# Kernel tuning notes

Measured on AMD Instinct MI355X. Metric: run time of the kernel, lower is better.

## Reference

```python
import jax, jax.numpy as jnp
import numpy as np

N = 10000   # num_nodes
F = 64      # latent_dim
U = 128     # num_units
B = 8       # batch
K = 2       # gcn_step
E = 160000  # edges (avg degree 16)
M = 2 * K + 1  # num_matrices = len(supports)*gcn_step + 1


def setup_inputs() -> dict:
    rng = np.random.default_rng(0)
    rows = rng.integers(0, N, E).astype(np.int32)
    cols = rng.integers(0, N, E).astype(np.int32)
    vals = (rng.random(E).astype(np.float32) + 0.1)
    # random-walk normalization D^{-1} A, per the original utils.calculate_random_walk_matrix
    deg_out = np.zeros(N, np.float32); np.add.at(deg_out, rows, vals)
    deg_in = np.zeros(N, np.float32); np.add.at(deg_in, cols, vals)
    # support1 = (D_out^{-1} A)^T : out[c] += vals/d_out[r] * x[r]  -> dst=cols, src=rows
    w1 = vals / np.maximum(deg_out[rows], 1e-8)
    # support2 = (D_in^{-1} A^T)^T : out[r] += vals/d_in[c] * x[c]  -> dst=rows, src=cols
    w2 = vals / np.maximum(deg_in[cols], 1e-8)

    key = jax.random.key(0)
    ks = jax.random.split(key, 4)

    def xavier(k, shape):
        std = (2.0 / (shape[0] + shape[1])) ** 0.5
        return jax.random.normal(k, shape, jnp.float32) * std

    return {
        'y': jax.random.normal(ks[0], (B, N * F), jnp.float32),
        'W_lat': xavier(ks[1], (M * F, F)),
        'b_lat': jnp.ones((F,), jnp.float32),   # bias_start=1.0, shared (keyed by length)
        'W_units': xavier(ks[2], (M * F, U)),
        'b_units': jnp.zeros((U,), jnp.float32),
        'W_final': xavier(ks[3], (M * U, F)),
        'sup1_w': jnp.asarray(w1),
        'sup2_w': jnp.asarray(w2),
        'edge_rows': jnp.asarray(rows),
        'edge_cols': jnp.asarray(cols),
    }


def _spmm(dst, src, w, x):
    # sparse matmul S @ x with S given as COO edge list; x: (N, Fin, B)
    return jax.ops.segment_sum(w[:, None, None] * x[src], dst, num_segments=N)


def _gconv(x, supports, W, b):
    # x: (B, N, Fin) -> (B, N*Fout); Chebyshev diffusion convolution
    Bsz, n, fin = x.shape
    x0 = jnp.transpose(x, (1, 2, 0))  # (N, Fin, B)
    xs = [x0]
    for dst, src, w in supports:
        xk_2 = x0
        x1 = _spmm(dst, src, w, x0)
        xs.append(x1)
        for _ in range(2, K + 1):
            x2 = 2.0 * _spmm(dst, src, w, x1) - xk_2
            xs.append(x2)
            xk_2, x1 = x1, x2
    X = jnp.stack(xs, axis=-1)                       # (N, Fin, B, M)
    X = jnp.transpose(X, (2, 0, 1, 3)).reshape(Bsz * n, fin * len(xs))  # feature-major, matrix-minor
    out = X @ W + b
    return out.reshape(Bsz, n * W.shape[1])


def reference(y, W_lat, b_lat, W_units, b_units, W_final, sup1_w, sup2_w, edge_rows, edge_cols):
    supports = [(edge_cols, edge_rows, sup1_w), (edge_rows, edge_cols, sup2_w)]
    x = y.reshape(B, N, F)
    # theta gate (bias_start=1.0 via shared b_lat)
    theta = jax.nn.sigmoid(_gconv(x, supports, W_lat, b_lat))
    # ode_func_net: gen_layers=1 hidden gconv + final gconv (final bias is shared b_lat!)
    c = jnp.tanh(_gconv(x, supports, W_units, b_units)).reshape(B, N, U)
    c = jnp.tanh(_gconv(c, supports, W_final, b_lat))
    return -theta * c
```

## Files before the change

kernel.cpp:

```cpp
#include <hip/hip_runtime.h>

#define N_NODES 10000
#define NEDGE 160000
#define NB 80000
#define EPAD (NEDGE + 8 * N_NODES)

typedef unsigned int u32;
typedef unsigned short u16;
typedef __attribute__((ext_vector_type(8))) short short8;
typedef __attribute__((ext_vector_type(4))) float float4v;

__device__ __forceinline__ u16 f2bf(float f) {
    u32 u = __float_as_uint(f);
    return (u16)((u + 0x7fffu + ((u >> 16) & 1u)) >> 16);
}
__device__ __forceinline__ float lo16(u32 u) { return __uint_as_float(u << 16); }
__device__ __forceinline__ float hi16(u32 u) { return __uint_as_float(u & 0xffff0000u); }
__device__ __forceinline__ u32 pack2(float a, float b) {
    return (u32)f2bf(a) | (((u32)f2bf(b)) << 16);
}
__device__ __forceinline__ float fast_tanh(float v) {
    return 1.f - 2.f / (__expf(2.f * v) + 1.f);
}

static const size_t SLAB = (size_t)NB * 64;

__global__ __launch_bounds__(256) void prepcount_kernel(
    const float2* __restrict__ y, u32* __restrict__ X0,
    const float* __restrict__ W_lat, const float* __restrict__ W_units,
    u16* __restrict__ bpk12, const float* __restrict__ W_final, u16* __restrict__ bpkP,
    const int* __restrict__ rows, const int* __restrict__ cols, int* __restrict__ cnt) {
    int b = blockIdx.x, t = threadIdx.x;
    if (b < 10000) {
        int idx = b * 256 + t;
        int fh = idx & 31;
        int rb = idx >> 5;
        int bb = rb & 7;
        int n = rb >> 3;
        float2 v = y[((size_t)bb * N_NODES + n) * 32 + fh];
        X0[idx] = pack2(v.x, v.y);
    } else if (b < 10240) {
        int idx = (b - 10000) * 256 + t;
        int j = idx & 7;
        int lane = (idx >> 3) & 63;
        int rest = idx >> 9;
        int ct = rest % 12;
        int ks = rest / 12;
        int k = ks * 32 + (lane >> 4) * 8 + j;
        int col = ct * 16 + (lane & 15);
        int wrow = (k % 64) * 5 + (k / 64);
        float v = (col < 64) ? W_lat[wrow * 64 + col] : W_units[wrow * 128 + (col - 64)];
        bpk12[idx] = f2bf(v);
    } else if (b < 10400) {
        int idx = (b - 10240) * 256 + t;
        int j8 = idx & 7;
        int lane = (idx >> 3) & 63;
        int rest = idx >> 9;
        int ct = rest % 20;
        int ks = rest / 20;
        int k = ks * 32 + (lane >> 4) * 8 + j8;
        int col = ct * 16 + (lane & 15);
        int slot = col >> 6, j = col & 63;
        float v;
        if (slot == 0)
            v = W_final[(k * 5 + 0) * 64 + j] - W_final[(k * 5 + 2) * 64 + j] -
                W_final[(k * 5 + 4) * 64 + j];
        else
            v = W_final[(k * 5 + slot) * 64 + j];
        bpkP[idx] = f2bf(v);
    } else {
        int e = (b - 10400) * 256 + t;
        atomicAdd(&cnt[cols[e]], 1);
        atomicAdd(&cnt[N_NODES + rows[e]], 1);
    }
}

__global__ void blocksum_kernel(const int* __restrict__ cnt, int* __restrict__ bsums) {
    __shared__ int red[4];
    int arr = blockIdx.x / 40;
    int c = blockIdx.x % 40;
    int idx = c * 256 + threadIdx.x;
    int v = (idx < N_NODES) ? ((cnt[arr * N_NODES + idx] + 7) & ~7) : 0;
#pragma unroll
    for (int off = 32; off; off >>= 1) v += __shfl_down(v, off, 64);
    int wv = threadIdx.x >> 6, ln = threadIdx.x & 63;
    if (ln == 0) red[wv] = v;
    __syncthreads();
    if (threadIdx.x == 0) bsums[blockIdx.x] = red[0] + red[1] + red[2] + red[3];
}

__global__ void scanapply_kernel(int* __restrict__ cnt, const int* __restrict__ bsums,
                                 int* __restrict__ rowptr1, int* __restrict__ rowptr2) {
    __shared__ int lds[256];
    int arr = blockIdx.x / 40;
    int c = blockIdx.x % 40;
    int base = 0;
    for (int i = 0; i < c; i++) base += bsums[arr * 40 + i];
    int idx = c * 256 + threadIdx.x;
    bool ok = idx < N_NODES;
    int v = ok ? ((cnt[arr * N_NODES + idx] + 7) & ~7) : 0;
    int t = threadIdx.x;
    lds[t] = v;
    __syncthreads();
    for (int off = 1; off < 256; off <<= 1) {
        int add = (t >= off) ? lds[t - off] : 0;
        __syncthreads();
        lds[t] += add;
        __syncthreads();
    }
    int excl = lds[t] - v + base;
    if (ok) {
        int* rp = arr ? rowptr2 : rowptr1;
        rp[idx] = excl;
        cnt[arr * N_NODES + idx] = excl;
    }
    if (c == 39 && t == 255) {
        (arr ? rowptr2 : rowptr1)[N_NODES] = base + lds[255];
    }
}

__global__ void scatter_kernel(const int* __restrict__ rows, const int* __restrict__ cols,
                               const float* __restrict__ w1, const float* __restrict__ w2,
                               int* __restrict__ cur1, int* __restrict__ cur2,
                               int2* __restrict__ edges1, int2* __restrict__ edges2) {
    int e = blockIdx.x * 256 + threadIdx.x;
    if (e < NEDGE) {
        int r = rows[e], c = cols[e];
        int p1 = atomicAdd(&cur1[c], 1);
        edges1[p1] = make_int2(r, __float_as_int(w1[e]));
        int p2 = atomicAdd(&cur2[r], 1);
        edges2[p2] = make_int2(c, __float_as_int(w2[e]));
    }
}

__device__ __forceinline__ void gacc(float* acc, float w, uint4 u) {
    acc[0] += w * lo16(u.x); acc[1] += w * hi16(u.x);
    acc[2] += w * lo16(u.y); acc[3] += w * hi16(u.y);
    acc[4] += w * lo16(u.z); acc[5] += w * hi16(u.z);
    acc[6] += w * lo16(u.w); acc[7] += w * hi16(u.w);
}

__device__ __forceinline__ void gather_sliced(const u32* __restrict__ Xin,
                                              const int* __restrict__ rp,
                                              const int2* __restrict__ eg,
                                              int row, bool valid, int su, int l,
                                              float* acc) {
    int e = 0, e1 = 0;
    if (valid) {
        e = rp[row] + l;
        e1 = rp[row + 1];
    }
    while (__ballot(e < e1)) {
        int2 me = make_int2(0, 0);
        if (e < e1) me = eg[e];
#pragma unroll
        for (int j = 0; j < 8; j++) {
            int s = __shfl(me.x, j, 8);
            float w = __int_as_float(__shfl(me.y, j, 8));
            uint4 u = *(const uint4*)(Xin + (size_t)s * 256 + su + l * 4);
            gacc(acc, w, u);
        }
        e += 8;
    }
}

__global__ __launch_bounds__(256) void spmm2_kernel(
    const u32* __restrict__ XinA, const u32* __restrict__ XprevA, u32* __restrict__ XoutA,
    const u32* __restrict__ XinB, const u32* __restrict__ XprevB, u32* __restrict__ XoutB,
    const int* __restrict__ rowptr1, const int2* __restrict__ edges1,
    const int* __restrict__ rowptr2, const int2* __restrict__ edges2,
    float alpha, float beta) {
    int t = threadIdx.x;
    int lane = t & 63;
    int g = lane >> 3, l = lane & 7;
    int slice = blockIdx.x & 7;
    int chunk = blockIdx.x >> 3;
    int su = slice * 32;
    int v = chunk * 32 + (t >> 6) * 8 + g;
    bool hB = v >= N_NODES;
    int n = hB ? v - N_NODES : v;
    const u32* Xin = hB ? XinB : XinA;
    const u32* Xprev = hB ? XprevB : XprevA;
    u32* Xout = hB ? XoutB : XoutA;
    const int* rp = hB ? rowptr2 : rowptr1;
    const int2* eg = hB ? edges2 : edges1;

    float acc[8] = {0.f, 0.f, 0.f, 0.f, 0.f, 0.f, 0.f, 0.f};
    gather_sliced(Xin, rp, eg, n, true, su, l, acc);

    size_t o = (size_t)n * 256 + su + l * 4;
    if (beta != 0.f) {
        uint4 p = *(const uint4*)(Xprev + o);
        acc[0] = alpha * acc[0] + beta * lo16(p.x); acc[1] = alpha * acc[1] + beta * hi16(p.x);
        acc[2] = alpha * acc[2] + beta * lo16(p.y); acc[3] = alpha * acc[3] + beta * hi16(p.y);
        acc[4] = alpha * acc[4] + beta * lo16(p.z); acc[5] = alpha * acc[5] + beta * hi16(p.z);
        acc[6] = alpha * acc[6] + beta * lo16(p.w); acc[7] = alpha * acc[7] + beta * hi16(p.w);
    } else {
#pragma unroll
        for (int i = 0; i < 8; i++) acc[i] *= alpha;
    }
    uint4 r;
    r.x = pack2(acc[0], acc[1]);
    r.y = pack2(acc[2], acc[3]);
    r.z = pack2(acc[4], acc[5]);
    r.w = pack2(acc[6], acc[7]);
    *(uint4*)(Xout + o) = r;
}

__global__ __launch_bounds__(256) void spmm_final_kernel(
    const u32* __restrict__ T1, const u32* __restrict__ T2,
    const u32* __restrict__ Q, const u32* __restrict__ theta,
    const int* __restrict__ rowptr1, const int2* __restrict__ edges1,
    const int* __restrict__ rowptr2, const int2* __restrict__ edges2,
    float* __restrict__ outF) {
    int t = threadIdx.x;
    int lane = t & 63;
    int g = lane >> 3, l = lane & 7;
    int slice = blockIdx.x & 7;
    int chunk = blockIdx.x >> 3;
    int su = slice * 32;
    int n = chunk * 32 + (t >> 6) * 8 + g;
    bool valid = n < N_NODES;

    float acc[8] = {0.f, 0.f, 0.f, 0.f, 0.f, 0.f, 0.f, 0.f};
    gather_sliced(T1, rowptr1, edges1, n, valid, su, l, acc);
    gather_sliced(T2, rowptr2, edges2, n, valid, su, l, acc);
    if (!valid) return;

    size_t o = (size_t)n * 256 + su + l * 4;
    uint4 q = *(const uint4*)(Q + o);
    uint4 th = *(const uint4*)(theta + o);
    float res[8];
    res[0] = -lo16(th.x) * fast_tanh(lo16(q.x) + acc[0]);
    res[1] = -hi16(th.x) * fast_tanh(hi16(q.x) + acc[1]);
    res[2] = -lo16(th.y) * fast_tanh(lo16(q.y) + acc[2]);
    res[3] = -hi16(th.y) * fast_tanh(hi16(q.y) + acc[3]);
    res[4] = -lo16(th.z) * fast_tanh(lo16(q.z) + acc[4]);
    res[5] = -hi16(th.z) * fast_tanh(hi16(q.z) + acc[5]);
    res[6] = -lo16(th.w) * fast_tanh(lo16(q.w) + acc[6]);
    res[7] = -hi16(th.w) * fast_tanh(hi16(q.w) + acc[7]);
    float* dst = outF + (size_t)slice * (N_NODES * 64) + (size_t)n * 64 + l * 8;
    *(float4*)(dst) = make_float4(res[0], res[1], res[2], res[3]);
    *(float4*)(dst + 4) = make_float4(res[4], res[5], res[6], res[7]);
}

struct Slabs { const u16* p[5]; };

template <int FIN, int NM, int NOUT, int CT, int MODE>
__global__ __launch_bounds__(256, 6) void gemm_kernel(
    Slabs A, const u16* __restrict__ Bp, const float* __restrict__ bias1,
    const float* __restrict__ bias2, u16* __restrict__ O1, u16* __restrict__ O2) {
    constexpr int K = NM * FIN;
    constexpr int KS = K / 32;
    constexpr int CTT = NOUT / 16;
    static_assert(CT * 4 == CTT, "4 waves cover all col tiles");

    int t = threadIdx.x;
    int lane = t & 63;
    int wave = t >> 6;
    int ctBase = wave * CT;
    int rowBase = blockIdx.x * 32;
    int mrow = lane & 15;
    int kq = lane >> 4;

    float4v acc0[CT], acc1[CT];
#pragma unroll
    for (int c = 0; c < CT; c++) {
        acc0[c] = (float4v){0.f, 0.f, 0.f, 0.f};
        acc1[c] = (float4v){0.f, 0.f, 0.f, 0.f};
    }

#pragma unroll
    for (int ks = 0; ks < KS; ks++) {
        int k = ks * 32 + kq * 8;
        int m = k / FIN;
        int koff = k % FIN;
        const u16* ap = A.p[m];
        short8 a0 = *(const short8*)(ap + (size_t)(rowBase + mrow) * FIN + koff);
        short8 a1 = *(const short8*)(ap + (size_t)(rowBase + 16 + mrow) * FIN + koff);
#pragma unroll
        for (int ct = 0; ct < CT; ct++) {
            short8 b = *(const short8*)(Bp +
                        ((size_t)(ks * CTT + ctBase + ct) * 64 + lane) * 8);
            acc0[ct] = __builtin_amdgcn_mfma_f32_16x16x32_bf16(b, a0, acc0[ct], 0, 0, 0);
            acc1[ct] = __builtin_amdgcn_mfma_f32_16x16x32_bf16(b, a1, acc1[ct], 0, 0, 0);
        }
    }

#pragma unroll
    for (int hr = 0; hr < 2; hr++) {
        size_t r = (size_t)(rowBase + hr * 16 + mrow);
#pragma unroll
        for (int ct = 0; ct < CT; ct++) {
            float4v av = hr ? acc1[ct] : acc0[ct];
            int col0 = (ctBase + ct) * 16 + kq * 4;
            float v[4];
#pragma unroll
            for (int i = 0; i < 4; i++) v[i] = av[i];
            if (MODE == 0) {
                if (col0 < 64) {
#pragma unroll
                    for (int i = 0; i < 4; i++) v[i] += bias1[col0 + i];
                }
                uint2 w = make_uint2(pack2(v[0], v[1]), pack2(v[2], v[3]));
                *(uint2*)(O1 + (size_t)(col0 >> 6) * SLAB + r * 64 + (col0 & 63)) = w;
            } else {
                if (col0 < 64) {
#pragma unroll
                    for (int i = 0; i < 4; i++)
                        v[i] = 1.f / (1.f + __expf(-(v[i] + bias1[col0 + i])));
                    uint2 w = make_uint2(pack2(v[0], v[1]), pack2(v[2], v[3]));
                    *(uint2*)(O1 + r * 64 + col0) = w;
                } else {
#pragma unroll
                    for (int i = 0; i < 4; i++)
                        v[i] = fast_tanh(v[i] + bias2[col0 - 64 + i]);
                    uint2 w = make_uint2(pack2(v[0], v[1]), pack2(v[2], v[3]));
                    *(uint2*)(O2 + r * 128 + (col0 - 64)) = w;
                }
            }
        }
    }
}

extern "C" void kernel_launch(void* const* d_in, const int* in_sizes, int n_in,
                              void* d_out, int out_size, void* d_ws, size_t ws_size,
                              hipStream_t stream) {
    const float2* y    = (const float2*)d_in[0];
    const float* W_lat = (const float*)d_in[1];
    const float* b_lat = (const float*)d_in[2];
    const float* W_units = (const float*)d_in[3];
    const float* b_units = (const float*)d_in[4];
    const float* W_final = (const float*)d_in[5];
    const float* sup1w = (const float*)d_in[6];
    const float* sup2w = (const float*)d_in[7];
    const int* rows    = (const int*)d_in[8];
    const int* cols    = (const int*)d_in[9];
    float* out = (float*)d_out;

    char* ws = (char*)d_ws;
    size_t off = 0;
    auto alloc = [&](size_t bytes) -> void* {
        void* p = ws + off;
        off += (bytes + 511) & ~(size_t)511;
        return p;
    };
    int* rowptr1 = (int*)alloc((N_NODES + 1) * 4);
    int* rowptr2 = (int*)alloc((N_NODES + 1) * 4);
    int* cnt = (int*)alloc((size_t)2 * N_NODES * 4);
    int* bsums = (int*)alloc(80 * 4);
    int2* edges1 = (int2*)alloc((size_t)EPAD * 8);
    int2* edges2 = (int2*)alloc((size_t)EPAD * 8);
    u16* bpk12 = (u16*)alloc((size_t)61440 * 2);
    u16* bpkP = (u16*)alloc((size_t)40960 * 2);
    u16* theta = (u16*)alloc((size_t)NB * 64 * 2);
    u16* S = (u16*)alloc((size_t)5 * NB * 64 * 2);
    u16* H0 = (u16*)alloc((size_t)NB * 128 * 2);
    u16* T1 = (u16*)alloc((size_t)NB * 64 * 2);
    u16* T2 = (u16*)alloc((size_t)NB * 64 * 2);

    hipMemsetAsync(cnt, 0, (size_t)2 * N_NODES * 4, stream);
    hipMemsetAsync(edges1, 0, (size_t)EPAD * 8, stream);
    hipMemsetAsync(edges2, 0, (size_t)EPAD * 8, stream);
    prepcount_kernel<<<11025, 256, 0, stream>>>(y, (u32*)S, W_lat, W_units, bpk12,
                                                W_final, bpkP, rows, cols, cnt);
    blocksum_kernel<<<80, 256, 0, stream>>>(cnt, bsums);
    scanapply_kernel<<<80, 256, 0, stream>>>(cnt, bsums, rowptr1, rowptr2);
    scatter_kernel<<<625, 256, 0, stream>>>(rows, cols, sup1w, sup2w,
                                            cnt, cnt + N_NODES, edges1, edges2);

    const u32* S0 = (const u32*)S;
    u32* X1 = (u32*)(S + 1 * SLAB);
    u32* X2 = (u32*)(S + 2 * SLAB);
    u32* X3 = (u32*)(S + 3 * SLAB);
    u32* X4 = (u32*)(S + 4 * SLAB);
    spmm2_kernel<<<5000, 256, 0, stream>>>(S0, nullptr, X1, S0, nullptr, X3,
                                           rowptr1, edges1, rowptr2, edges2, 1.f, 0.f);
    spmm2_kernel<<<5000, 256, 0, stream>>>(X1, S0, X2, X3, S0, X4,
                                           rowptr1, edges1, rowptr2, edges2, 2.f, -1.f);

    Slabs SX;
    for (int m = 0; m < 5; m++) SX.p[m] = S + (size_t)m * SLAB;
    gemm_kernel<64, 5, 192, 3, 1><<<2500, 256, 0, stream>>>(SX, bpk12, b_lat, b_units, theta, H0);

    Slabs SH;
    SH.p[0] = H0;
    gemm_kernel<128, 1, 320, 5, 0><<<2500, 256, 0, stream>>>(SH, bpkP, b_lat, nullptr, S, nullptr);

    const u32* Q  = (const u32*)(S + 0 * SLAB);
    const u32* P1 = (const u32*)(S + 1 * SLAB);
    const u32* P2 = (const u32*)(S + 2 * SLAB);
    const u32* P3 = (const u32*)(S + 3 * SLAB);
    const u32* P4 = (const u32*)(S + 4 * SLAB);
    spmm2_kernel<<<5000, 256, 0, stream>>>(P2, P1, (u32*)T1, P4, P3, (u32*)T2,
                                           rowptr1, edges1, rowptr2, edges2, 2.f, 1.f);
    spmm_final_kernel<<<2504, 256, 0, stream>>>((const u32*)T1, (const u32*)T2, Q,
                                                (const u32*)theta,
                                                rowptr1, edges1, rowptr2, edges2, out);
}
```

Measured before the change: 334.7 us.

## Restructure GEMM to 16-row tiles with preloaded A and prefetched B fragments

The GEMM kernel now handles 16 rows per block instead of 32, which doubles the grid to 5000 blocks. It preloads every A fragment into registers up front and double-buffers the B fragment loads one k-step ahead of the MFMAs. Launch bounds drop from 6 to 4 blocks per CU to leave room for the larger register footprint. The aim is more parallelism and latency hiding, at the cost of halving B-fragment reuse (each B load now feeds one MFMA instead of two) and lowering occupancy.

Result: slower. 342.7 us (+2.4%).

```diff
diff --git a/kernel.cpp b/kernel.cpp
--- a/kernel.cpp
+++ b/kernel.cpp
@@ -247,77 +247,82 @@
 struct Slabs { const u16* p[5]; };
 
 template <int FIN, int NM, int NOUT, int CT, int MODE>
-__global__ __launch_bounds__(256, 6) void gemm_kernel(
+__global__ __launch_bounds__(256, 4) void gemm_kernel(
     Slabs A, const u16* __restrict__ Bp, const float* __restrict__ bias1,
     const float* __restrict__ bias2, u16* __restrict__ O1, u16* __restrict__ O2) {
     constexpr int K = NM * FIN;
     constexpr int KS = K / 32;
     constexpr int CTT = NOUT / 16;
-    static_assert(CT * 4 == CTT, "4 waves cover all col tiles");
+    static_assert(CT * 4 == CTT, "4 waves = 4 col groups");
 
     int t = threadIdx.x;
     int lane = t & 63;
     int wave = t >> 6;
     int ctBase = wave * CT;
-    int rowBase = blockIdx.x * 32;
+    size_t rowBase = (size_t)blockIdx.x * 16;
     int mrow = lane & 15;
     int kq = lane >> 4;
 
-    float4v acc0[CT], acc1[CT];
-#pragma unroll
-    for (int c = 0; c < CT; c++) {
-        acc0[c] = (float4v){0.f, 0.f, 0.f, 0.f};
-        acc1[c] = (float4v){0.f, 0.f, 0.f, 0.f};
-    }
-
+    short8 a[KS];
 #pragma unroll
     for (int ks = 0; ks < KS; ks++) {
         int k = ks * 32 + kq * 8;
-        int m = k / FIN;
-        int koff = k % FIN;
-        const u16* ap = A.p[m];
-        short8 a0 = *(const short8*)(ap + (size_t)(rowBase + mrow) * FIN + koff);
-        short8 a1 = *(const short8*)(ap + (size_t)(rowBase + 16 + mrow) * FIN + koff);
-#pragma unroll
-        for (int ct = 0; ct < CT; ct++) {
-            short8 b = *(const short8*)(Bp +
-                        ((size_t)(ks * CTT + ctBase + ct) * 64 + lane) * 8);
-            acc0[ct] = __builtin_amdgcn_mfma_f32_16x16x32_bf16(b, a0, acc0[ct], 0, 0, 0);
-            acc1[ct] = __builtin_amdgcn_mfma_f32_16x16x32_bf16(b, a1, acc1[ct], 0, 0, 0);
+        a[ks] = *(const short8*)(A.p[k / FIN] + (rowBase + mrow) * FIN + (k % FIN));
+    }
+
+    float4v acc[CT];
+#pragma unroll
+    for (int c = 0; c < CT; c++) acc[c] = (float4v){0.f, 0.f, 0.f, 0.f};
+
+    short8 bc[CT];
+#pragma unroll
+    for (int ct = 0; ct < CT; ct++)
+        bc[ct] = *(const short8*)(Bp + ((size_t)(ctBase + ct) * 64 + lane) * 8);
+#pragma unroll
+    for (int ks = 0; ks < KS; ks++) {
+        short8 bn[CT];
+        if (ks + 1 < KS) {
+#pragma unroll
+            for (int ct = 0; ct < CT; ct++)
+                bn[ct] = *(const short8*)(Bp +
+                          ((size_t)((ks + 1) * CTT + ctBase + ct) * 64 + lane) * 8);
         }
-    }
-
-#pragma unroll
-    for (int hr = 0; hr < 2; hr++) {
-        size_t r = (size_t)(rowBase + hr * 16 + mrow);
-#pragma unroll
-        for (int ct = 0; ct < CT; ct++) {
-            float4v av = hr ? acc1[ct] : acc0[ct];
-            int col0 = (ctBase + ct) * 16 + kq * 4;
-            float v[4];
-#pragma unroll
-            for (int i = 0; i < 4; i++) v[i] = av[i];
-            if (MODE == 0) {
-                if (col0 < 64) {
-#pragma unroll
-                    for (int i = 0; i < 4; i++) v[i] += bias1[col0 + i];
-                }
+#pragma unroll
+        for (int ct = 0; ct < CT; ct++)
+            acc[ct] = __builtin_amdgcn_mfma_f32_16x16x32_bf16(bc[ct], a[ks], acc[ct], 0, 0, 0);
+        if (ks + 1 < KS) {
+#pragma unroll
+            for (int ct = 0; ct < CT; ct++) bc[ct] = bn[ct];
+        }
+    }
+
+    size_t r = rowBase + mrow;
+#pragma unroll
+    for (int ct = 0; ct < CT; ct++) {
+        int col0 = (ctBase + ct) * 16 + kq * 4;
+        float v[4];
+#pragma unroll
+        for (int i = 0; i < 4; i++) v[i] = acc[ct][i];
+        if (MODE == 0) {
+            if (col0 < 64) {
+#pragma unroll
+                for (int i = 0; i < 4; i++) v[i] += bias1[col0 + i];
+            }
+            uint2 w = make_uint2(pack2(v[0], v[1]), pack2(v[2], v[3]));
+            *(uint2*)(O1 + (size_t)(col0 >> 6) * SLAB + r * 64 + (col0 & 63)) = w;
+        } else {
+            if (col0 < 64) {
+#pragma unroll
+                for (int i = 0; i < 4; i++)
+                    v[i] = 1.f / (1.f + __expf(-(v[i] + bias1[col0 + i])));
                 uint2 w = make_uint2(pack2(v[0], v[1]), pack2(v[2], v[3]));
-                *(uint2*)(O1 + (size_t)(col0 >> 6) * SLAB + r * 64 + (col0 & 63)) = w;
+                *(uint2*)(O1 + r * 64 + col0) = w;
             } else {
-                if (col0 < 64) {
-#pragma unroll
-                    for (int i = 0; i < 4; i++)
-                        v[i] = 1.f / (1.f + __expf(-(v[i] + bias1[col0 + i])));
-                    uint2 w = make_uint2(pack2(v[0], v[1]), pack2(v[2], v[3]));
-                    *(uint2*)(O1 + r * 64 + col0) = w;
-                } else {
-#pragma unroll
-                    for (int i = 0; i < 4; i++)
-                        v[i] = fast_tanh(v[i] + bias2[col0 - 64 + i]);
-                    uint2 w = make_uint2(pack2(v[0], v[1]), pack2(v[2], v[3]));
-                    *(uint2*)(O2 + r * 128 + (col0 - 64)) = w;
-                }
+#pragma unroll
+                for (int i = 0; i < 4; i++)
+                    v[i] = fast_tanh(v[i] + bias2[col0 - 64 + i]);
+                uint2 w = make_uint2(pack2(v[0], v[1]), pack2(v[2], v[3]));
+                *(uint2*)(O2 + r * 128 + (col0 - 64)) = w;
             }
         }
     }
@@ -381,11 +386,11 @@
 
     Slabs SX;
     for (int m = 0; m < 5; m++) SX.p[m] = S + (size_t)m * SLAB;
-    gemm_kernel<64, 5, 192, 3, 1><<<2500, 256, 0, stream>>>(SX, bpk12, b_lat, b_units, theta, H0);
+    gemm_kernel<64, 5, 192, 3, 1><<<5000, 256, 0, stream>>>(SX, bpk12, b_lat, b_units, theta, H0);
 
     Slabs SH;
     SH.p[0] = H0;
-    gemm_kernel<128, 1, 320, 5, 0><<<2500, 256, 0, stream>>>(SH, bpkP, b_lat, nullptr, S, nullptr);
+    gemm_kernel<128, 1, 320, 5, 0><<<5000, 256, 0, stream>>>(SH, bpkP, b_lat, nullptr, S, nullptr);
 
     const u32* Q  = (const u32*)(S + 0 * SLAB);
     const u32* P1 = (const u32*)(S + 1 * SLAB);
```
